# Kernel optimization log

Measured on AMD Instinct MI355X. Metric: run time of the kernel, lower is better.

The kernel has to match this reference:

```python
import jax, jax.numpy as jnp
import numpy as np

OUTPUT_DIM = 1024
D_K = 1024  # Lt feature dim
D_Q = 1024  # rnn_ht feature dim
SCALE = 1.0 / np.sqrt(64.0)  # hardcoded 64**0.5 in original, NOT sqrt(output_dim)


def setup_inputs() -> dict:
    key = jax.random.key(0)
    k1, k2, k3, k4 = jax.random.split(key, 4)
    B, Sq, Sk = 8, 2048, 2048
    Lt = jax.random.normal(k1, (B, Sk, D_K), dtype=jnp.float32)
    rnn_ht = jax.random.normal(k2, (B, Sq, D_Q), dtype=jnp.float32)
    # 'uniform' keras initializer: U(-0.05, 0.05)
    kernel = jax.random.uniform(k3, (2, D_K, OUTPUT_DIM), dtype=jnp.float32, minval=-0.05, maxval=0.05)
    W = jax.random.uniform(k4, (D_Q, OUTPUT_DIM), dtype=jnp.float32, minval=-0.05, maxval=0.05)
    return {"Lt": Lt, "rnn_ht": rnn_ht, "kernel": kernel, "W": W}


def reference(Lt, rnn_ht, kernel, W):
    WQ = jnp.einsum('bsd,de->bse', rnn_ht, W)          # [B, Sq, E]
    WK = jnp.einsum('bsd,de->bse', Lt, kernel[0])      # [B, Sk, E]
    WV = jnp.einsum('bsd,de->bse', Lt, kernel[1])      # [B, Sk, E]
    QK = jnp.einsum('bqe,bke->bqk', WQ, WK) * SCALE    # [B, Sq, Sk]
    weights = jax.nn.softmax(QK, axis=-1)
    context_vector = jnp.einsum('bqk,bke->bqe', weights, WV)  # [B, Sq, E]
    return (context_vector, weights)
```

## Files before the change

### kernel.cpp

```cpp
#include <hip/hip_runtime.h>


typedef __bf16 bf16x8 __attribute__((ext_vector_type(8)));
typedef __bf16 bf16x4 __attribute__((ext_vector_type(4)));
typedef float  f32x4  __attribute__((ext_vector_type(4)));

__device__ __forceinline__ void gload_lds16(const void* g, void* l) {
  __builtin_amdgcn_global_load_lds(
      (__attribute__((address_space(1))) void*)(g),
      (__attribute__((address_space(3))) void*)(uintptr_t)(l),
      16, 0, 0);
}

__device__ __forceinline__ int swz(int r, int g) {
  return r * 64 + ((g ^ (r & 7)) << 3);
}

template <bool OUTBF16>
__global__ __launch_bounds__(256)
void gemm_nt(const __bf16* __restrict__ Ap, const __bf16* __restrict__ Bp,
             void* __restrict__ Cp, int N, int K,
             unsigned long long sAb, unsigned long long sBb,
             unsigned long long sCb, float scale) {
  __shared__ __bf16 As[128 * 64];
  __shared__ __bf16 Bs[128 * 64];

  const int tid  = threadIdx.x;
  const int wave = tid >> 6;
  const int lane = tid & 63;
  const int wm   = (wave >> 1) * 64;
  const int wn   = (wave & 1) * 64;

  int bx, by, bz;
  {
    const int nx = gridDim.x, ny = gridDim.y;
    const int d = blockIdx.x + nx * (blockIdx.y + ny * blockIdx.z);
    if (gridDim.z == 8 && ((nx * ny) & 63) == 0 && (nx & 7) == 0) {
      bz = d & 7;
      const int s = d >> 3;
      const int sq = s >> 6, w = s & 63;
      const int nsx = nx >> 3;
      const int sqx = sq % nsx, sqy = sq / nsx;
      bx = sqx * 8 + (w & 7);
      by = sqy * 8 + (w >> 3);
    } else {
      bx = blockIdx.x; by = blockIdx.y; bz = blockIdx.z;
    }
  }
  const size_t m0 = (size_t)by * 128;
  const size_t n0 = (size_t)bx * 128;
  const __bf16* Ab = Ap + (size_t)bz * sAb;
  const __bf16* Bb = Bp + (size_t)bz * sBb;

  f32x4 acc[4][4] = {};
  const int fm = lane & 15;

  for (int kt = 0; kt < K; kt += 64) {
#pragma unroll
    for (int i = 0; i < 4; ++i) {
      const int c = wave * 4 + i;
      const int r = c * 8 + (lane >> 3);
      const int g = (lane & 7) ^ (r & 7);
      gload_lds16(Ab + (m0 + r) * (size_t)K + kt + g * 8, &As[c * 512]);
    }
#pragma unroll
    for (int i = 0; i < 4; ++i) {
      const int c = wave * 4 + i;
      const int r = c * 8 + (lane >> 3);
      const int g = (lane & 7) ^ (r & 7);
      gload_lds16(Bb + (n0 + r) * (size_t)K + kt + g * 8, &Bs[c * 512]);
    }
    __syncthreads();

#pragma unroll
    for (int h = 0; h < 2; ++h) {
      const int gq = (lane >> 4) + h * 4;
      bf16x8 afr[4], bfr[4];
#pragma unroll
      for (int i = 0; i < 4; ++i)
        afr[i] = *(const bf16x8*)&As[swz(wm + i * 16 + fm, gq)];
#pragma unroll
      for (int j = 0; j < 4; ++j)
        bfr[j] = *(const bf16x8*)&Bs[swz(wn + j * 16 + fm, gq)];
#pragma unroll
      for (int i = 0; i < 4; ++i)
#pragma unroll
        for (int j = 0; j < 4; ++j)
          acc[i][j] = __builtin_amdgcn_mfma_f32_16x16x32_bf16(
              afr[i], bfr[j], acc[i][j], 0, 0, 0);
    }
    __syncthreads();
  }

  const int col   = lane & 15;
  const int rquad = (lane >> 4) * 4;
#pragma unroll
  for (int i = 0; i < 4; ++i) {
#pragma unroll
    for (int r = 0; r < 4; ++r) {
      const size_t row = m0 + wm + i * 16 + rquad + r;
#pragma unroll
      for (int j = 0; j < 4; ++j) {
        const size_t cidx = (size_t)bz * sCb + row * (size_t)N + n0 + wn + j * 16 + col;
        if constexpr (OUTBF16) {
          ((__bf16*)Cp)[cidx] = (__bf16)acc[i][j][r];
        } else {
          ((float*)Cp)[cidx] = acc[i][j][r] * scale;
        }
      }
    }
  }
}

__global__ __launch_bounds__(256)
void cvt_transpose(const float* __restrict__ s0, const float* __restrict__ s1,
                   const float* __restrict__ s2, __bf16* __restrict__ d0,
                   __bf16* __restrict__ d1, __bf16* __restrict__ d2) {
  const float* s = blockIdx.z == 0 ? s0 : (blockIdx.z == 1 ? s1 : s2);
  __bf16* d      = blockIdx.z == 0 ? d0 : (blockIdx.z == 1 ? d1 : d2);
  __shared__ float tile[32][33];
  const int x  = blockIdx.x * 32 + threadIdx.x;
  const int y0 = blockIdx.y * 32;
  for (int j = threadIdx.y; j < 32; j += 8)
    tile[j][threadIdx.x] = s[(size_t)(y0 + j) * 1024 + x];
  __syncthreads();
  const int x2 = y0 + threadIdx.x;
  const int y2 = blockIdx.x * 32;
  for (int j = threadIdx.y; j < 32; j += 8)
    d[(size_t)(y2 + j) * 1024 + x2] = (__bf16)tile[threadIdx.x][j];
}

__global__ __launch_bounds__(256)
void cvt_bf16(const float* __restrict__ s0, __bf16* __restrict__ d0,
              const float* __restrict__ s1, __bf16* __restrict__ d1) {
  const float* s = blockIdx.z ? s1 : s0;
  __bf16* d      = blockIdx.z ? d1 : d0;
  const size_t i = ((size_t)blockIdx.x * 256 + threadIdx.x) * 4;
  float4 f = *(const float4*)(s + i);
  bf16x4 h = {(__bf16)f.x, (__bf16)f.y, (__bf16)f.z, (__bf16)f.w};
  *(bf16x4*)(d + i) = h;
}

__global__ __launch_bounds__(256)
void softmax_rows(float* __restrict__ Wt, __bf16* __restrict__ Pb) {
  const int t = threadIdx.x;
  float* p = Wt + (size_t)blockIdx.x * 2048;
  float4 a = ((float4*)p)[t];
  float4 b = ((float4*)p)[t + 256];

  float m = fmaxf(fmaxf(fmaxf(a.x, a.y), fmaxf(a.z, a.w)),
                  fmaxf(fmaxf(b.x, b.y), fmaxf(b.z, b.w)));
#pragma unroll
  for (int off = 32; off > 0; off >>= 1) m = fmaxf(m, __shfl_xor(m, off));
  __shared__ float red[8];
  if ((t & 63) == 0) red[t >> 6] = m;
  __syncthreads();
  m = fmaxf(fmaxf(red[0], red[1]), fmaxf(red[2], red[3]));

  a.x = __expf(a.x - m); a.y = __expf(a.y - m);
  a.z = __expf(a.z - m); a.w = __expf(a.w - m);
  b.x = __expf(b.x - m); b.y = __expf(b.y - m);
  b.z = __expf(b.z - m); b.w = __expf(b.w - m);
  float s = a.x + a.y + a.z + a.w + b.x + b.y + b.z + b.w;
#pragma unroll
  for (int off = 32; off > 0; off >>= 1) s += __shfl_xor(s, off);
  if ((t & 63) == 0) red[4 + (t >> 6)] = s;
  __syncthreads();
  s = red[4] + red[5] + red[6] + red[7];

  const float inv = 1.0f / s;
  a.x *= inv; a.y *= inv; a.z *= inv; a.w *= inv;
  b.x *= inv; b.y *= inv; b.z *= inv; b.w *= inv;
  ((float4*)p)[t] = a;
  ((float4*)p)[t + 256] = b;

  __bf16* pb = Pb + (size_t)blockIdx.x * 2048;
  bf16x4 ha = {(__bf16)a.x, (__bf16)a.y, (__bf16)a.z, (__bf16)a.w};
  bf16x4 hb = {(__bf16)b.x, (__bf16)b.y, (__bf16)b.z, (__bf16)b.w};
  *(bf16x4*)(pb + (size_t)t * 4) = ha;
  *(bf16x4*)(pb + (size_t)(t + 256) * 4) = hb;
}

extern "C" void kernel_launch(void* const* d_in, const int* in_sizes, int n_in,
                              void* d_out, int out_size, void* d_ws,
                              size_t ws_size, hipStream_t stream) {
  const float* Lt  = (const float*)d_in[0];
  const float* rnn = (const float*)d_in[1];
  const float* ker = (const float*)d_in[2];
  const float* W   = (const float*)d_in[3];

  float* ctx = (float*)d_out;
  float* wts = ctx + (size_t)16777216;

  __bf16* ws   = (__bf16*)d_ws;
  __bf16* Wt   = ws;
  __bf16* k0t  = Wt + (1u << 20);
  __bf16* k1t  = k0t + (1u << 20);
  __bf16* WQ   = k1t + (1u << 20);
  __bf16* WK   = WQ + (16u << 20);
  __bf16* WVt  = WK + (16u << 20);
  __bf16* Ltb  = WVt + (16u << 20);
  __bf16* rnnb = Ltb + (16u << 20);
  __bf16* Pb = Ltb;

  cvt_transpose<<<dim3(32, 32, 3), dim3(32, 8), 0, stream>>>(
      W, ker, ker + (1u << 20), Wt, k0t, k1t);

  cvt_bf16<<<dim3(16384, 1, 2), 256, 0, stream>>>(Lt, Ltb, rnn, rnnb);

  gemm_nt<true><<<dim3(8, 128, 1), 256, 0, stream>>>(
      rnnb, Wt, WQ, 1024, 1024, 0ull, 0ull, 0ull, 1.0f);
  gemm_nt<true><<<dim3(8, 128, 1), 256, 0, stream>>>(
      Ltb, k0t, WK, 1024, 1024, 0ull, 0ull, 0ull, 1.0f);

  gemm_nt<true><<<dim3(16, 8, 8), 256, 0, stream>>>(
      k1t, Ltb, WVt, 2048, 1024, 0ull, 2048ull * 1024ull,
      1024ull * 2048ull, 1.0f);

  gemm_nt<false><<<dim3(16, 16, 8), 256, 0, stream>>>(
      WQ, WK, wts, 2048, 1024, 2048ull * 1024ull, 2048ull * 1024ull,
      2048ull * 2048ull, 0.125f);

  softmax_rows<<<16384, 256, 0, stream>>>(wts, Pb);

  gemm_nt<false><<<dim3(8, 16, 8), 256, 0, stream>>>(
      Pb, WVt, ctx, 1024, 2048, 2048ull * 2048ull, 1024ull * 2048ull,
      2048ull * 1024ull, 1.0f);
}
```

Baseline: 672.1 us.

## Rewrite GEMM as 256x256-tile, 8-wave kernel with multi-buffered ping-pong LDS pipeline

Replaces the 128x128 single-stage GEMM with a 256x256 tile computed by 512 threads (8 waves, each owning 128x64), using 128 KB of LDS split into two k-stages of two 32-wide halves. Global-to-LDS loads for future k-slices are issued in between MFMA phases, with explicit vmcnt waits, s_barrier, sched_barrier and setprio, so that memory traffic overlaps compute. The block-to-tile mapping is also changed to spread consecutive blocks across XCDs. The cost targeted is the load-then-compute serialization and the low arithmetic intensity of the old kernel. In exchange it brings high register pressure from the 8x4 accumulators, a hard assumption that K is a multiple of 128, and fewer, larger blocks, which may reduce occupancy and leave part of the GPU idle on the smaller GEMMs.

```diff
diff --git a/kernel.cpp b/kernel.cpp
--- a/kernel.cpp
+++ b/kernel.cpp
@@ -12,104 +12,187 @@
       16, 0, 0);
 }
 
-__device__ __forceinline__ int swz(int r, int g) {
-  return r * 64 + ((g ^ (r & 7)) << 3);
-}
+__device__ __forceinline__ void ldfrag4(bf16x8 (&f)[4], const __bf16* reg_,
+                                        int rbase, int fm, int gq) {
+#pragma unroll
+  for (int i = 0; i < 4; ++i) {
+    const int r = rbase + i * 16 + fm;
+    f[i] = *(const bf16x8*)(reg_ + r * 32 + ((gq ^ ((r >> 1) & 3)) << 3));
+  }
+}
+
+__device__ __forceinline__ void stage16(const __bf16* src, __bf16* dst,
+                                        size_t rowstride, int wave, int lane) {
+#pragma unroll
+  for (int i = 0; i < 2; ++i) {
+    const int chunk = wave * 2 + i;
+    const int row = chunk * 16 + (lane >> 2);
+    const int gg = (lane & 3) ^ ((row >> 1) & 3);
+    gload_lds16(src + (size_t)row * rowstride + (gg << 3), dst + chunk * 512);
+  }
+}
+
+template <int MH>
+__device__ __forceinline__ void mfma16(f32x4 (&acc)[8][4], const bf16x8 (&a)[4],
+                                       const bf16x8 (&b)[4]) {
+#pragma unroll
+  for (int mi = 0; mi < 4; ++mi)
+#pragma unroll
+    for (int nj = 0; nj < 4; ++nj)
+      acc[MH * 4 + mi][nj] = __builtin_amdgcn_mfma_f32_16x16x32_bf16(
+          a[mi], b[nj], acc[MH * 4 + mi][nj], 0, 0, 0);
+}
+
+#define PHASE_MID()                       \
+  __builtin_amdgcn_sched_barrier(0);      \
+  __builtin_amdgcn_s_barrier();           \
+  __builtin_amdgcn_s_setprio(1)
+
+#define PHASE_END()                       \
+  __builtin_amdgcn_s_setprio(0);          \
+  __builtin_amdgcn_sched_barrier(0);      \
+  __builtin_amdgcn_s_barrier()
 
 template <bool OUTBF16>
-__global__ __launch_bounds__(256)
+__global__ __launch_bounds__(512, 2)
 void gemm_nt(const __bf16* __restrict__ Ap, const __bf16* __restrict__ Bp,
              void* __restrict__ Cp, int N, int K,
              unsigned long long sAb, unsigned long long sBb,
              unsigned long long sCb, float scale) {
-  __shared__ __bf16 As[128 * 64];
-  __shared__ __bf16 Bs[128 * 64];
+  __shared__ __bf16 lds[65536];
 
   const int tid  = threadIdx.x;
   const int wave = tid >> 6;
   const int lane = tid & 63;
-  const int wm   = (wave >> 1) * 64;
-  const int wn   = (wave & 1) * 64;
+  const int wm   = (wave >> 2) * 128;
+  const int wn   = (wave & 3) * 64;
+  const int fm   = lane & 15;
+  const int gq   = lane >> 4;
 
   int bx, by, bz;
   {
     const int nx = gridDim.x, ny = gridDim.y;
     const int d = blockIdx.x + nx * (blockIdx.y + ny * blockIdx.z);
-    if (gridDim.z == 8 && ((nx * ny) & 63) == 0 && (nx & 7) == 0) {
+    if (gridDim.z == 8) {
       bz = d & 7;
       const int s = d >> 3;
-      const int sq = s >> 6, w = s & 63;
-      const int nsx = nx >> 3;
-      const int sqx = sq % nsx, sqy = sq / nsx;
-      bx = sqx * 8 + (w & 7);
-      by = sqy * 8 + (w >> 3);
+      bx = s % nx; by = s / nx;
     } else {
-      bx = blockIdx.x; by = blockIdx.y; bz = blockIdx.z;
+      const int cpx = (nx * ny) >> 3;
+      const int s = (d & 7) * cpx + (d >> 3);
+      bx = s % nx; by = s / nx; bz = 0;
     }
   }
-  const size_t m0 = (size_t)by * 128;
-  const size_t n0 = (size_t)bx * 128;
-  const __bf16* Ab = Ap + (size_t)bz * sAb;
-  const __bf16* Bb = Bp + (size_t)bz * sBb;
-
-  f32x4 acc[4][4] = {};
-  const int fm = lane & 15;
-
-  for (int kt = 0; kt < K; kt += 64) {
-#pragma unroll
-    for (int i = 0; i < 4; ++i) {
-      const int c = wave * 4 + i;
-      const int r = c * 8 + (lane >> 3);
-      const int g = (lane & 7) ^ (r & 7);
-      gload_lds16(Ab + (m0 + r) * (size_t)K + kt + g * 8, &As[c * 512]);
-    }
-#pragma unroll
-    for (int i = 0; i < 4; ++i) {
-      const int c = wave * 4 + i;
-      const int r = c * 8 + (lane >> 3);
-      const int g = (lane & 7) ^ (r & 7);
-      gload_lds16(Bb + (n0 + r) * (size_t)K + kt + g * 8, &Bs[c * 512]);
-    }
-    __syncthreads();
-
-#pragma unroll
-    for (int h = 0; h < 2; ++h) {
-      const int gq = (lane >> 4) + h * 4;
-      bf16x8 afr[4], bfr[4];
-#pragma unroll
-      for (int i = 0; i < 4; ++i)
-        afr[i] = *(const bf16x8*)&As[swz(wm + i * 16 + fm, gq)];
-#pragma unroll
-      for (int j = 0; j < 4; ++j)
-        bfr[j] = *(const bf16x8*)&Bs[swz(wn + j * 16 + fm, gq)];
-#pragma unroll
-      for (int i = 0; i < 4; ++i)
-#pragma unroll
-        for (int j = 0; j < 4; ++j)
-          acc[i][j] = __builtin_amdgcn_mfma_f32_16x16x32_bf16(
-              afr[i], bfr[j], acc[i][j], 0, 0, 0);
-    }
-    __syncthreads();
+  const size_t m0 = (size_t)by * 256;
+  const size_t n0 = (size_t)bx * 256;
+  const __bf16* Aa = Ap + (size_t)bz * sAb + m0 * (size_t)K;
+  const __bf16* Ba = Bp + (size_t)bz * sBb + n0 * (size_t)K;
+
+  __bf16* const As_ = lds;
+  __bf16* const Bs_ = lds + 32768;
+#define AREG(p, h) (As_ + (p) * 16384 + (h) * 8192)
+#define BREG(p, h) (Bs_ + (p) * 16384 + (h) * 8192)
+
+  f32x4 acc[8][4] = {};
+  bf16x8 a[4], b[4];
+
+  stage16(Ba + 0,  BREG(0, 0), K, wave, lane);
+  stage16(Aa + 0,  AREG(0, 0), K, wave, lane);
+  stage16(Ba + 32, BREG(0, 1), K, wave, lane);
+  stage16(Aa + 32, AREG(0, 1), K, wave, lane);
+  asm volatile("s_waitcnt vmcnt(4)" ::: "memory");
+  stage16(Ba + 64, BREG(1, 0), K, wave, lane);
+  stage16(Aa + 64, AREG(1, 0), K, wave, lane);
+  stage16(Ba + 96, BREG(1, 1), K, wave, lane);
+  asm volatile("s_waitcnt vmcnt(6)" ::: "memory");
+  __builtin_amdgcn_s_barrier();
+
+  const int niter = K >> 7;
+  for (int it = 0; it < niter; ++it) {
+    const int kt = it << 7;
+    const bool s2 = (kt + 128) < K;
+
+    ldfrag4(a, AREG(0, 0), wm, fm, gq);
+    ldfrag4(b, BREG(0, 0), wn, fm, gq);
+    stage16(Aa + kt + 96, AREG(1, 1), K, wave, lane);
+    PHASE_MID();
+    mfma16<0>(acc, a, b);
+    PHASE_END();
+
+    ldfrag4(a, AREG(0, 0), wm + 64, fm, gq);
+    if (s2) stage16(Ba + kt + 128, BREG(0, 0), K, wave, lane);
+    PHASE_MID();
+    mfma16<1>(acc, a, b);
+    PHASE_END();
+
+    ldfrag4(a, AREG(0, 1), wm, fm, gq);
+    ldfrag4(b, BREG(0, 1), wn, fm, gq);
+    if (s2) stage16(Aa + kt + 128, AREG(0, 0), K, wave, lane);
+    PHASE_MID();
+    mfma16<0>(acc, a, b);
+    PHASE_END();
+
+    ldfrag4(a, AREG(0, 1), wm + 64, fm, gq);
+    if (s2) stage16(Ba + kt + 160, BREG(0, 1), K, wave, lane);
+    PHASE_MID();
+    mfma16<1>(acc, a, b);
+    __builtin_amdgcn_s_setprio(0);
+    __builtin_amdgcn_sched_barrier(0);
+    if (s2) { asm volatile("s_waitcnt vmcnt(6)" ::: "memory"); }
+    else    { asm volatile("s_waitcnt vmcnt(0)" ::: "memory"); }
+    __builtin_amdgcn_s_barrier();
+
+    ldfrag4(a, AREG(1, 0), wm, fm, gq);
+    ldfrag4(b, BREG(1, 0), wn, fm, gq);
+    if (s2) stage16(Aa + kt + 160, AREG(0, 1), K, wave, lane);
+    PHASE_MID();
+    mfma16<0>(acc, a, b);
+    PHASE_END();
+
+    ldfrag4(a, AREG(1, 0), wm + 64, fm, gq);
+    if (s2) stage16(Ba + kt + 192, BREG(1, 0), K, wave, lane);
+    PHASE_MID();
+    mfma16<1>(acc, a, b);
+    PHASE_END();
+
+    ldfrag4(a, AREG(1, 1), wm, fm, gq);
+    ldfrag4(b, BREG(1, 1), wn, fm, gq);
+    if (s2) stage16(Aa + kt + 192, AREG(1, 0), K, wave, lane);
+    PHASE_MID();
+    mfma16<0>(acc, a, b);
+    PHASE_END();
+
+    ldfrag4(a, AREG(1, 1), wm + 64, fm, gq);
+    if (s2) stage16(Ba + kt + 224, BREG(1, 1), K, wave, lane);
+    PHASE_MID();
+    mfma16<1>(acc, a, b);
+    __builtin_amdgcn_s_setprio(0);
+    __builtin_amdgcn_sched_barrier(0);
+    if (s2) { asm volatile("s_waitcnt vmcnt(6)" ::: "memory"); }
+    __builtin_amdgcn_s_barrier();
   }
 
   const int col   = lane & 15;
   const int rquad = (lane >> 4) * 4;
 #pragma unroll
-  for (int i = 0; i < 4; ++i) {
+  for (int mi = 0; mi < 8; ++mi) {
 #pragma unroll
     for (int r = 0; r < 4; ++r) {
-      const size_t row = m0 + wm + i * 16 + rquad + r;
-#pragma unroll
-      for (int j = 0; j < 4; ++j) {
-        const size_t cidx = (size_t)bz * sCb + row * (size_t)N + n0 + wn + j * 16 + col;
+      const size_t row = m0 + wm + mi * 16 + rquad + r;
+#pragma unroll
+      for (int nj = 0; nj < 4; ++nj) {
+        const size_t cidx =
+            (size_t)bz * sCb + row * (size_t)N + n0 + wn + nj * 16 + col;
         if constexpr (OUTBF16) {
-          ((__bf16*)Cp)[cidx] = (__bf16)acc[i][j][r];
+          ((__bf16*)Cp)[cidx] = (__bf16)acc[mi][nj][r];
         } else {
-          ((float*)Cp)[cidx] = acc[i][j][r] * scale;
+          ((float*)Cp)[cidx] = acc[mi][nj][r] * scale;
         }
       }
     }
   }
+#undef AREG
+#undef BREG
 }
 
 __global__ __launch_bounds__(256)
@@ -208,22 +291,22 @@
 
   cvt_bf16<<<dim3(16384, 1, 2), 256, 0, stream>>>(Lt, Ltb, rnn, rnnb);
 
-  gemm_nt<true><<<dim3(8, 128, 1), 256, 0, stream>>>(
+  gemm_nt<true><<<dim3(4, 64, 1), 512, 0, stream>>>(
       rnnb, Wt, WQ, 1024, 1024, 0ull, 0ull, 0ull, 1.0f);
-  gemm_nt<true><<<dim3(8, 128, 1), 256, 0, stream>>>(
+  gemm_nt<true><<<dim3(4, 64, 1), 512, 0, stream>>>(
       Ltb, k0t, WK, 1024, 1024, 0ull, 0ull, 0ull, 1.0f);
 
-  gemm_nt<true><<<dim3(16, 8, 8), 256, 0, stream>>>(
+  gemm_nt<true><<<dim3(8, 4, 8), 512, 0, stream>>>(
       k1t, Ltb, WVt, 2048, 1024, 0ull, 2048ull * 1024ull,
       1024ull * 2048ull, 1.0f);
 
-  gemm_nt<false><<<dim3(16, 16, 8), 256, 0, stream>>>(
+  gemm_nt<false><<<dim3(8, 8, 8), 512, 0, stream>>>(
       WQ, WK, wts, 2048, 1024, 2048ull * 1024ull, 2048ull * 1024ull,
       2048ull * 2048ull, 0.125f);
 
   softmax_rows<<<16384, 256, 0, stream>>>(wts, Pb);
 
-  gemm_nt<false><<<dim3(8, 16, 8), 256, 0, stream>>>(
+  gemm_nt<false><<<dim3(4, 8, 8), 512, 0, stream>>>(
       Pb, WVt, ctx, 1024, 2048, 2048ull * 2048ull, 1024ull * 2048ull,
       2048ull * 1024ull, 1.0f);
 }
```

Measured after the change: 584.4 us. 1.15x faster.
